# Kernel tuning notes

Measured on AMD Instinct MI355X. Metric: run time of the kernel, lower is better.

Reference implementation:

```python
import jax, jax.numpy as jnp
import numpy as np

O_H, O_W = 7, 7  # crop size (init output_shape)


def setup_inputs() -> dict:
    key = jax.random.key(0)
    k1, k2 = jax.random.split(key)
    fmaps = jax.random.normal(k1, (8, 128, 128, 256), dtype=jnp.float32)
    rois = jax.random.uniform(k2, (8, 128, 4), dtype=jnp.float32)  # (x1,y1,x2,y2) in [0,1]
    return {"fmaps": fmaps, "rois": rois}


def _roi_align_single(fmap, rois, o_h, o_w):
    """fmap: [H,W,C], rois: [N,4] (x1,y1,x2,y2) fractional. Replicates
    tf.image.crop_and_resize(bilinear) after the module's box rescaling."""
    H, W, C = fmap.shape
    Hf = jnp.float32(H)
    Wf = jnp.float32(W)
    # module: scale to pixel coords by (W,H), reorder to (y1,x1,y2,x2), divide by (dim-1)
    by1 = rois[:, 1] * Hf / (Hf - 1.0)
    bx1 = rois[:, 0] * Wf / (Wf - 1.0)
    by2 = rois[:, 3] * Hf / (Hf - 1.0)
    bx2 = rois[:, 2] * Wf / (Wf - 1.0)
    i = jnp.arange(o_h, dtype=jnp.float32)
    j = jnp.arange(o_w, dtype=jnp.float32)
    # crop_and_resize sampling grid (crop size > 1 branch)
    in_y = by1[:, None] * (Hf - 1.0) + i[None, :] * ((by2 - by1)[:, None] * (Hf - 1.0) / (o_h - 1))  # [N,o_h]
    in_x = bx1[:, None] * (Wf - 1.0) + j[None, :] * ((bx2 - bx1)[:, None] * (Wf - 1.0) / (o_w - 1))  # [N,o_w]
    valid_y = (in_y >= 0.0) & (in_y <= Hf - 1.0)
    valid_x = (in_x >= 0.0) & (in_x <= Wf - 1.0)
    in_y = jnp.clip(in_y, 0.0, Hf - 1.0)
    in_x = jnp.clip(in_x, 0.0, Wf - 1.0)
    y0 = jnp.floor(in_y)
    x0 = jnp.floor(in_x)
    ly = in_y - y0  # [N,o_h]
    lx = in_x - x0  # [N,o_w]
    y0i = y0.astype(jnp.int32)
    x0i = x0.astype(jnp.int32)
    y1i = jnp.minimum(y0i + 1, H - 1)
    x1i = jnp.minimum(x0i + 1, W - 1)
    # corner gathers -> [N,o_h,o_w,C]
    tl = fmap[y0i[:, :, None], x0i[:, None, :]]
    tr = fmap[y0i[:, :, None], x1i[:, None, :]]
    bl = fmap[y1i[:, :, None], x0i[:, None, :]]
    br = fmap[y1i[:, :, None], x1i[:, None, :]]
    lxb = lx[:, None, :, None]
    top = tl + (tr - tl) * lxb
    bot = bl + (br - bl) * lxb
    out = top + (bot - top) * ly[:, :, None, None]
    # crop_and_resize extrapolation_value = 0 outside the image
    mask = (valid_y[:, :, None] & valid_x[:, None, :]).astype(out.dtype)
    return out * mask[..., None]


def reference(fmaps, rois):
    # [B,N,o_h,o_w,C]
    return jax.vmap(lambda f, r: _roi_align_single(f, r, O_H, O_W))(fmaps, rois)
```

## Files before the change

kernel.cpp:

```cpp
#include <hip/hip_runtime.h>


#define NBATCH 8
#define NROI   128
#define FH     128
#define FW     128
#define NC     256
#define OH     7
#define OW     7

typedef float f32x4 __attribute__((ext_vector_type(4)));

__global__ __launch_bounds__(256) void roi_align_kernel(
    const float* __restrict__ fmaps,
    const float* __restrict__ rois,
    float* __restrict__ out)
{
    const int nb8 = gridDim.x >> 3;
    const int blk = (blockIdx.x & 7) * nb8 + (blockIdx.x >> 3);

    const int lane = threadIdx.x & 63;
    const int pix = __builtin_amdgcn_readfirstlane((blk * 256 + (int)threadIdx.x) >> 6);

    const int j   = pix % OW;
    int t         = pix / OW;
    const int i   = t % OH;
    t             = t / OH;
    const int roi = t % NROI;
    const int b   = t / NROI;

    const float* r = rois + (size_t)(b * NROI + roi) * 4;
    const float x1 = r[0], y1 = r[1], x2 = r[2], y2 = r[3];

    const float Hf = 128.0f, Wf = 128.0f;
    const float by1 = y1 * Hf / (Hf - 1.0f);
    const float bx1 = x1 * Wf / (Wf - 1.0f);
    const float by2 = y2 * Hf / (Hf - 1.0f);
    const float bx2 = x2 * Wf / (Wf - 1.0f);

    float in_y = by1 * (Hf - 1.0f) + (float)i * ((by2 - by1) * (Hf - 1.0f) / 6.0f);
    float in_x = bx1 * (Wf - 1.0f) + (float)j * ((bx2 - bx1) * (Wf - 1.0f) / 6.0f);

    const bool valid = (in_y >= 0.0f) & (in_y <= Hf - 1.0f) &
                       (in_x >= 0.0f) & (in_x <= Wf - 1.0f);

    in_y = fminf(fmaxf(in_y, 0.0f), Hf - 1.0f);
    in_x = fminf(fmaxf(in_x, 0.0f), Wf - 1.0f);

    const float y0f = floorf(in_y);
    const float x0f = floorf(in_x);
    const float ly  = in_y - y0f;
    const float lx  = in_x - x0f;
    const int y0  = (int)y0f;
    const int x0  = (int)x0f;
    const int y1i = min(y0 + 1, FH - 1);
    const int x1i = min(x0 + 1, FW - 1);

    const f32x4* __restrict__ f =
        (const f32x4*)(fmaps + (size_t)b * FH * FW * NC);

    const f32x4 tl = f[(y0  * FW + x0 ) * 64 + lane];
    const f32x4 tr = f[(y0  * FW + x1i) * 64 + lane];
    const f32x4 bl = f[(y1i * FW + x0 ) * 64 + lane];
    const f32x4 br = f[(y1i * FW + x1i) * 64 + lane];

    const float m = valid ? 1.0f : 0.0f;

    const f32x4 top = tl + (tr - tl) * lx;
    const f32x4 bot = bl + (br - bl) * lx;
    const f32x4 o   = (top + (bot - top) * ly) * m;

    f32x4* op = (f32x4*)out + (size_t)pix * 64 + lane;
    __builtin_nontemporal_store(o, op);
}

extern "C" void kernel_launch(void* const* d_in, const int* in_sizes, int n_in,
                              void* d_out, int out_size, void* d_ws, size_t ws_size,
                              hipStream_t stream) {
    const float* fmaps = (const float*)d_in[0];
    const float* rois  = (const float*)d_in[1];
    float* out = (float*)d_out;

    const int total = NBATCH * NROI * OH * OW * 64;
    roi_align_kernel<<<total / 256, 256, 0, stream>>>(fmaps, rois, out);
}
```

Baseline: 200.6 us.

## Process a full output row per wavefront with batched corner loads

Each wavefront now computes all seven output columns of one crop row instead of one pixel. The y-interpolation setup and ROI reads are shared across the row, and the corner loads for four and then three columns are issued together before any math to raise memory-level parallelism. The grid shrinks by a factor of seven and the XCD-aware block remapping is dropped. The trade is higher register use and fewer wavefronts in flight, plus possible loss of L2 locality from removing the swizzle.

```diff
diff --git a/kernel.cpp b/kernel.cpp
--- a/kernel.cpp
+++ b/kernel.cpp
@@ -11,21 +11,52 @@
 
 typedef float f32x4 __attribute__((ext_vector_type(4)));
 
+template<int N>
+__device__ __forceinline__ void do_chunk(
+    int j0, float in_x0, float dxw, bool vy, float ly,
+    const f32x4* __restrict__ r0, const f32x4* __restrict__ r1,
+    int lane, f32x4* __restrict__ ob)
+{
+    f32x4 tl[N], tr[N], bl[N], br[N];
+    float lx[N], m[N];
+
+#pragma unroll
+    for (int k = 0; k < N; ++k) {
+        const int j = j0 + k;
+        float in_x = in_x0 + (float)j * dxw;
+        const bool vx = (in_x >= 0.0f) & (in_x <= 127.0f);
+        in_x = fminf(fmaxf(in_x, 0.0f), 127.0f);
+        const float x0f = floorf(in_x);
+        lx[k] = in_x - x0f;
+        const int x0  = (int)x0f;
+        const int x1i = min(x0 + 1, FW - 1);
+        tl[k] = r0[x0  * 64 + lane];
+        tr[k] = r0[x1i * 64 + lane];
+        bl[k] = r1[x0  * 64 + lane];
+        br[k] = r1[x1i * 64 + lane];
+        m[k] = (vy & vx) ? 1.0f : 0.0f;
+    }
+
+#pragma unroll
+    for (int k = 0; k < N; ++k) {
+        const f32x4 top = tl[k] + (tr[k] - tl[k]) * lx[k];
+        const f32x4 bot = bl[k] + (br[k] - bl[k]) * lx[k];
+        const f32x4 o   = (top + (bot - top) * ly) * m[k];
+        __builtin_nontemporal_store(o, ob + (size_t)(j0 + k) * 64 + lane);
+    }
+}
+
 __global__ __launch_bounds__(256) void roi_align_kernel(
     const float* __restrict__ fmaps,
     const float* __restrict__ rois,
     float* __restrict__ out)
 {
-    const int nb8 = gridDim.x >> 3;
-    const int blk = (blockIdx.x & 7) * nb8 + (blockIdx.x >> 3);
+    const int lane = threadIdx.x & 63;
+    const int row = __builtin_amdgcn_readfirstlane(
+        (int)blockIdx.x * 4 + ((int)threadIdx.x >> 6));
 
-    const int lane = threadIdx.x & 63;
-    const int pix = __builtin_amdgcn_readfirstlane((blk * 256 + (int)threadIdx.x) >> 6);
-
-    const int j   = pix % OW;
-    int t         = pix / OW;
-    const int i   = t % OH;
-    t             = t / OH;
+    const int i   = row % OH;
+    int t         = row / OH;
     const int roi = t % NROI;
     const int b   = t / NROI;
 
@@ -39,39 +70,26 @@
     const float bx2 = x2 * Wf / (Wf - 1.0f);
 
     float in_y = by1 * (Hf - 1.0f) + (float)i * ((by2 - by1) * (Hf - 1.0f) / 6.0f);
-    float in_x = bx1 * (Wf - 1.0f) + (float)j * ((bx2 - bx1) * (Wf - 1.0f) / 6.0f);
-
-    const bool valid = (in_y >= 0.0f) & (in_y <= Hf - 1.0f) &
-                       (in_x >= 0.0f) & (in_x <= Wf - 1.0f);
-
+    const bool vy = (in_y >= 0.0f) & (in_y <= Hf - 1.0f);
     in_y = fminf(fmaxf(in_y, 0.0f), Hf - 1.0f);
-    in_x = fminf(fmaxf(in_x, 0.0f), Wf - 1.0f);
 
     const float y0f = floorf(in_y);
-    const float x0f = floorf(in_x);
     const float ly  = in_y - y0f;
-    const float lx  = in_x - x0f;
-    const int y0  = (int)y0f;
-    const int x0  = (int)x0f;
-    const int y1i = min(y0 + 1, FH - 1);
-    const int x1i = min(x0 + 1, FW - 1);
+    const int   y0  = (int)y0f;
+    const int   y1i = min(y0 + 1, FH - 1);
+
+    const float in_x0 = bx1 * (Wf - 1.0f);
+    const float dxw   = (bx2 - bx1) * (Wf - 1.0f) / 6.0f;
 
     const f32x4* __restrict__ f =
         (const f32x4*)(fmaps + (size_t)b * FH * FW * NC);
+    const f32x4* __restrict__ r0 = f + (size_t)y0  * FW * 64;
+    const f32x4* __restrict__ r1 = f + (size_t)y1i * FW * 64;
 
-    const f32x4 tl = f[(y0  * FW + x0 ) * 64 + lane];
-    const f32x4 tr = f[(y0  * FW + x1i) * 64 + lane];
-    const f32x4 bl = f[(y1i * FW + x0 ) * 64 + lane];
-    const f32x4 br = f[(y1i * FW + x1i) * 64 + lane];
+    f32x4* __restrict__ ob = (f32x4*)out + (size_t)row * OW * 64;
 
-    const float m = valid ? 1.0f : 0.0f;
-
-    const f32x4 top = tl + (tr - tl) * lx;
-    const f32x4 bot = bl + (br - bl) * lx;
-    const f32x4 o   = (top + (bot - top) * ly) * m;
-
-    f32x4* op = (f32x4*)out + (size_t)pix * 64 + lane;
-    __builtin_nontemporal_store(o, op);
+    do_chunk<4>(0, in_x0, dxw, vy, ly, r0, r1, lane, ob);
+    do_chunk<3>(4, in_x0, dxw, vy, ly, r0, r1, lane, ob);
 }
 
 extern "C" void kernel_launch(void* const* d_in, const int* in_sizes, int n_in,
@@ -81,6 +99,6 @@
     const float* rois  = (const float*)d_in[1];
     float* out = (float*)d_out;
 
-    const int total = NBATCH * NROI * OH * OW * 64;
-    roi_align_kernel<<<total / 256, 256, 0, stream>>>(fmaps, rois, out);
+    const int rows = NBATCH * NROI * OH;
+    roi_align_kernel<<<rows / 4, 256, 0, stream>>>(fmaps, rois, out);
 }
```

Result: no change. 200.1 us, median of 2 (-0.3%).
